# Optimization experiments

Hardware: AMD Instinct MI355X
Metric: run time of the kernel (lower is better)

## Reference

```python
import jax, jax.numpy as jnp
import numpy as np

N_ROOMS = 128
N = 2 + N_ROOMS          # 2 external wall nodes + room nodes
T = 131072               # number of evaluation times
DT = 30.0                # seconds between evaluations
Q_LIM = 500.0
K_SCALE = 1e-5           # physical scaling of sigmoid(params) -> conductances [1/s]
DAY = 86400.0
TOUT_N = 1100            # hourly outside-temperature table covering the horizon


def setup_inputs() -> dict:
    key = jax.random.key(0)
    k1, k2, k3, k4 = jax.random.split(key, 4)
    t_eval = jnp.arange(T, dtype=jnp.float32) * DT
    params = jax.random.uniform(k1, (N * N,), dtype=jnp.float32)      # torch.rand init
    heating = jax.random.normal(k2, (N_ROOMS, 3), dtype=jnp.float32)  # torch.randn init
    B = jnp.zeros((N, 1 + N_ROOMS), dtype=jnp.float32)
    B = B.at[:, 0].set(jax.random.uniform(k3, (N,), dtype=jnp.float32) * 1e-5)  # Tout coupling
    B = B.at[2:, 1:].set(jnp.eye(N_ROOMS, dtype=jnp.float32) * 1e-6)           # heat input per room
    tout_t = jnp.arange(TOUT_N, dtype=jnp.float32) * 3600.0
    tout_v = 10.0 + 5.0 * jax.random.normal(k4, (TOUT_N,), dtype=jnp.float32)
    return {"t_eval": t_eval, "params": params, "heating": heating, "B": B,
            "tout_t": tout_t, "tout_v": tout_v}


def _forward(t_eval, params, heating, B, tout_t, tout_v):
    # transform + physical scaling of parameters -> RC conductance matrix A
    theta = jax.nn.sigmoid(params) * K_SCALE
    K = theta.reshape(N, N)
    d = jnp.diag(K)
    Koff = K - jnp.diag(d)
    A = Koff - jnp.diag(Koff.sum(axis=1) + d)   # Metzler, nonpositive row sums -> stable

    # transform + heat scaling -> continuous heating profile Qrms_continuous
    Q_avg = jax.nn.sigmoid(heating[:, 0]) * Q_LIM
    phase = heating[:, 1]
    sharp = heating[:, 2]

    t0 = t_eval[0]
    te = t_eval - t0
    two_pi = 2.0 * jnp.pi

    def Tout(t):  # Tout_continuous (linear interp, like scipy interp1d)
        return jnp.interp(t + t0, tout_t, tout_v)

    def Qf(t):    # smooth periodic heating schedule per room
        return Q_avg * jax.nn.sigmoid(sharp * jnp.sin(two_pi * (t + t0) / DAY + phase))

    def f(t, x):  # dx/dt = A @ x + B @ u
        u = jnp.concatenate([Tout(t)[None], Qf(t)])[:, None]   # [1+R, 1]
        return A @ x + B @ u

    iv = (Tout(te[0]) + 4.0) * jnp.ones((N, 1), dtype=jnp.float32)

    def step(x, tt):  # one RK4 step between consecutive evaluation times
        t, dt = tt
        half = dt * 0.5
        k1 = f(t, x)
        k2 = f(t + half, x + half * k1)
        k3 = f(t + half, x + half * k2)
        k4 = f(t + dt, x + dt * k3)
        xn = x + (dt / 6.0) * (k1 + 2.0 * k2 + 2.0 * k3 + k4)
        return xn, xn

    ts = te[:-1]
    dts = te[1:] - te[:-1]
    _, xs = jax.lax.scan(step, iv, (ts, dts))
    sol = jnp.concatenate([iv[None], xs], axis=0)   # [T, N, 1]
    return sol[:, 2:]                               # room temperatures only


def reference(t_eval, params, heating, B, tout_t, tout_v):
    return _forward(t_eval, params, heating, B, tout_t, tout_v)
```

## Files before the change

kernel.cpp:

```cpp
#include <hip/hip_runtime.h>
#include <math.h>

#define NPAD 132
#define TSTEPS 131071
#define LCH 128
#define NCH 1024
#define PERIOD 2880
#define OMEGA 7.2722052166430399e-05f

#define OFF_A    0
#define OFF_A2   17160
#define OFF_A3   34320
#define OFF_M    51480
#define OFF_C1   68640
#define OFF_C2   85800
#define OFF_P1   102960
#define OFF_P2   120120
#define OFF_M2   137280
#define OFF_M4   154440
#define OFF_M64  171600
#define OFF_M128 188760
#define OFF_M2K  205920
#define OFF_C1T  223080
#define OFF_C2T  239464
#define OFF_C1B  255848
#define OFF_C2B  255978
#define OFF_C3B  256108
#define OFF_AMP  256238
#define OFF_CPH  256366
#define OFF_SPH  256494
#define OFF_SH   256622
#define OFF_W    256750
#define OFF_G    257920
#define OFF_S64  391040
#define OFF_XB   524160
#define OFF_XB2  657280
#define OFF_SA   923520
#define OFF_GP   931710
#define OFF_GP2  1306110
#define OFF_GP4  1680510
#define OFF_TT   2054910

typedef float f4 __attribute__((ext_vector_type(4)));

#define MLOAD(Q, S) asm volatile("global_load_dwordx4 %0, %1, off offset:" S \
                                 : "=v"(mr[Q]) : "v"(base))
__device__ __forceinline__ void load_mrow(const float* base, f4* mr) {
    MLOAD(0, "0");    MLOAD(1, "16");   MLOAD(2, "32");   MLOAD(3, "48");
    MLOAD(4, "64");   MLOAD(5, "80");   MLOAD(6, "96");   MLOAD(7, "112");
    MLOAD(8, "128");  MLOAD(9, "144");  MLOAD(10, "160"); MLOAD(11, "176");
    MLOAD(12, "192"); MLOAD(13, "208"); MLOAD(14, "224"); MLOAD(15, "240");
    MLOAD(16, "256"); MLOAD(17, "272"); MLOAD(18, "288"); MLOAD(19, "304");
    MLOAD(20, "320"); MLOAD(21, "336"); MLOAD(22, "352"); MLOAD(23, "368");
    MLOAD(24, "384"); MLOAD(25, "400"); MLOAD(26, "416"); MLOAD(27, "432");
    MLOAD(28, "448"); MLOAD(29, "464"); MLOAD(30, "480"); MLOAD(31, "496");
    MLOAD(32, "512");
    asm volatile("s_waitcnt vmcnt(0)" ::: "memory");
    __builtin_amdgcn_sched_barrier(0);
}

__device__ __forceinline__ float sigm(float x) { return 1.0f / (1.0f + expf(-x)); }

__device__ __forceinline__ float interp_tout(float t, const float* __restrict__ tv) {
    float u = t * (1.0f / 3600.0f);
    int idx = (int)u;
    if (idx > 1098) idx = 1098;
    float fr = u - (float)idx;
    float v0 = tv[idx];
    return v0 + fr * (tv[idx + 1] - v0);
}

__global__ __launch_bounds__(256) void build_A_kernel(
    const float* __restrict__ params, const float* __restrict__ heating,
    const float* __restrict__ Bm, const float* __restrict__ tout_v,
    float* __restrict__ ws, float* __restrict__ out) {
    const int tid = threadIdx.x;
    float* A = ws + OFF_A;

    for (int idx = tid; idx < 130 * 130; idx += 256) {
        int r = idx / 130, c = idx - r * 130;
        A[r * NPAD + c] = sigm(params[idx]) * 1e-5f;
    }
    for (int r = tid; r < 130; r += 256) { A[r * NPAD + 130] = 0.f; A[r * NPAD + 131] = 0.f; }
    __syncthreads();
    for (int r = tid; r < 130; r += 256) {
        float s = 0.0f;
        for (int k = 0; k < 130; ++k) s += A[r * NPAD + k];
        A[r * NPAD + r] = -s;
    }
    for (int i = tid; i < 128; i += 256) {
        float bd = Bm[(2 + i) * 129 + (1 + i)];
        ws[OFF_AMP + i] = sigm(heating[i * 3]) * 500.0f * bd;
        float ph = heating[i * 3 + 1];
        ws[OFF_CPH + i] = cosf(ph);
        ws[OFF_SPH + i] = sinf(ph);
        ws[OFF_SH + i]  = heating[i * 3 + 2];
    }
    float iv = tout_v[0] + 4.0f;
    for (int i = tid; i < 128; i += 256) out[i] = iv;
    for (int r = tid; r < 130; r += 256) ws[OFF_XB + r] = iv;
}

__global__ __launch_bounds__(192) void mm_kernel(float* __restrict__ ws,
                                                 int offD, int offX, int offY) {
    const float* X = ws + offX;
    const float* Y = ws + offY;
    float* dst = ws + offD;
    __shared__ float xrow[130];
    const int r = blockIdx.x;
    const int c = threadIdx.x;
    if (c < 130) xrow[c] = X[r * NPAD + c];
    __syncthreads();
    if (c < 130) {
        float acc = 0.0f;
#pragma unroll 10
        for (int k = 0; k < 130; ++k)
            acc = fmaf(xrow[k], Y[k * NPAD + c], acc);
        dst[r * NPAD + c] = acc;
    }
    if (c >= 130 && c < 132) dst[r * NPAD + c] = 0.0f;
}

__global__ __launch_bounds__(192) void mm34_kernel(float* __restrict__ ws) {
    const int b = blockIdx.x;
    const bool hi = (b >= 130);
    const int r = hi ? b - 130 : b;
    const float* X = ws + (hi ? OFF_A2 : OFF_A);
    const float* Y = ws + OFF_A2;
    float* dst = ws + (hi ? OFF_P2 : OFF_A3);
    __shared__ float xrow[130];
    const int c = threadIdx.x;
    if (c < 130) xrow[c] = X[r * NPAD + c];
    __syncthreads();
    if (c < 130) {
        float acc = 0.0f;
#pragma unroll 10
        for (int k = 0; k < 130; ++k)
            acc = fmaf(xrow[k], Y[k * NPAD + c], acc);
        dst[r * NPAD + c] = acc;
    }
    if (c >= 130 && c < 132) dst[r * NPAD + c] = 0.0f;
}

__global__ __launch_bounds__(256) void combine_kernel(float* __restrict__ ws) {
    int idx = blockIdx.x * 256 + threadIdx.x;
    if (idx >= 130 * 130) return;
    int r = idx / 130, c = idx - r * 130;
    int o = r * NPAD + c;
    const float* A  = ws + OFF_A;
    const float* A2 = ws + OFF_A2;
    const float* A3 = ws + OFF_A3;
    const float* A4 = ws + OFF_P2;
    float eye = (r == c) ? 1.0f : 0.0f;
    float a = A[o], a2 = A2[o], a3 = A3[o], a4 = A4[o];
    float c1v = 5.0f * eye + 150.0f * a + 2250.0f * a2 + 33750.0f * a3;
    float c2v = 20.0f * eye + 300.0f * a + 2250.0f * a2;
    ws[OFF_M  + o] = eye + 30.0f * a + 450.0f * a2 + 4500.0f * a3 + 33750.0f * a4;
    ws[OFF_C1 + o] = c1v;
    ws[OFF_C2 + o] = c2v;
    if (r >= 2 && c >= 2) {
        ws[OFF_C1T + (c - 2) * 128 + (r - 2)] = c1v;
        ws[OFF_C2T + (c - 2) * 128 + (r - 2)] = c2v;
    }
    if (c == 0) {
        ws[OFF_M + r * NPAD + 130] = 0.f; ws[OFF_M + r * NPAD + 131] = 0.f;
        ws[OFF_C1 + r * NPAD + 130] = 0.f; ws[OFF_C1 + r * NPAD + 131] = 0.f;
        ws[OFF_C2 + r * NPAD + 130] = 0.f; ws[OFF_C2 + r * NPAD + 131] = 0.f;
    }
}

__global__ __launch_bounds__(192) void vecs2_kernel(const float* __restrict__ Bm,
                                                    float* __restrict__ ws) {
    const int r = threadIdx.x;
    const float* C1 = ws + OFF_C1;
    const float* C2 = ws + OFF_C2;
    const float* Mm = ws + OFF_M;
    __shared__ __align__(16) float va[132], vb[132], vd[132];
    __shared__ __align__(16) float na[132], nb[132], nd[132];
    __shared__ float a1s[130], a2s[130], c1bs[130];

    if (r < 132) { va[r] = 0.f; vb[r] = 0.f; vd[r] = 0.f; na[r] = 0.f; nb[r] = 0.f; nd[r] = 0.f; }
    __syncthreads();
    if (r < 130) {
        float s1 = 0.0f, s2 = 0.0f;
        for (int k = 0; k < 130; ++k) {
            float b0 = Bm[k * 129];
            s1 = fmaf(C1[r * NPAD + k], b0, s1);
            s2 = fmaf(C2[r * NPAD + k], b0, s2);
        }
        float c3 = 5.0f * Bm[r * 129];
        ws[OFF_C1B + r] = s1; ws[OFF_C2B + r] = s2; ws[OFF_C3B + r] = c3;
        ws[OFF_W + 7 * 130 + r] = s2;
        ws[OFF_W + 8 * 130 + r] = c3;
        va[r] = s1; vb[r] = s2; vd[r] = c3; c1bs[r] = s1;
    }
    __syncthreads();

    for (int st = 1; st <= 3; ++st) {
        if (r < 130) {
            const f4* mp = reinterpret_cast<const f4*>(&Mm[r * NPAD]);
            const f4* pa = reinterpret_cast<const f4*>(va);
            const f4* pb = reinterpret_cast<const f4*>(vb);
            const f4* pd = reinterpret_cast<const f4*>(vd);
            float aa = 0.f, ab = 0.f, ad = 0.f;
#pragma unroll
            for (int q = 0; q < 33; ++q) {
                f4 m = mp[q];
                f4 xa = pa[q], xb = pb[q], xd = pd[q];
                aa = fmaf(m.x, xa.x, fmaf(m.y, xa.y, fmaf(m.z, xa.z, fmaf(m.w, xa.w, aa))));
                ab = fmaf(m.x, xb.x, fmaf(m.y, xb.y, fmaf(m.z, xb.z, fmaf(m.w, xb.w, ab))));
                ad = fmaf(m.x, xd.x, fmaf(m.y, xd.y, fmaf(m.z, xd.z, fmaf(m.w, xd.w, ad))));
            }
            na[r] = aa; nb[r] = ab; nd[r] = ad;
        }
        __syncthreads();
        if (r < 130) {
            if (st == 1) { ws[OFF_W + 5 * 130 + r] = nb[r]; ws[OFF_W + 6 * 130 + r] = nd[r] + c1bs[r]; a1s[r] = na[r]; }
            if (st == 2) { ws[OFF_W + 3 * 130 + r] = nb[r]; ws[OFF_W + 4 * 130 + r] = nd[r] + a1s[r]; a2s[r] = na[r]; }
            if (st == 3) { ws[OFF_W + 0 * 130 + r] = na[r]; ws[OFF_W + 1 * 130 + r] = nb[r]; ws[OFF_W + 2 * 130 + r] = nd[r] + a2s[r]; }
            va[r] = na[r]; vb[r] = nb[r]; vd[r] = nd[r];
        }
        __syncthreads();
    }
}

__global__ __launch_bounds__(256) void gper_kernel(float* __restrict__ ws) {
    const int tid = threadIdx.x;
    const int n0 = blockIdx.x * 32;
    const float* C1T = ws + OFF_C1T;
    const float* C2T = ws + OFF_C2T;
    const float* C1 = ws + OFF_C1;
    const float* C2 = ws + OFF_C2;
    const float* amp = ws + OFF_AMP;
    const float* cph = ws + OFF_CPH;
    const float* sph = ws + OFF_SPH;
    const float* sh  = ws + OFF_SH;
    float* P = ws + OFF_GP;

    __shared__ __align__(16) float qgT[128][36];
    __shared__ __align__(16) float qmT[128][36];
    __shared__ float sth[65], cth[65];

    for (int j = tid; j < 65; j += 256) {
        float t = (j < 33) ? (float)(n0 + j) * 30.0f
                           : (float)(n0 + j - 33) * 30.0f + 15.0f;
        float a = t * OMEGA;
        sth[j] = sinf(a);
        cth[j] = cosf(a);
    }
    __syncthreads();

    for (int p = tid; p < 65 * 128; p += 256) {
        int j = p >> 7, i = p & 127;
        float s = sth[j] * cph[i] + cth[j] * sph[i];
        float v = amp[i] / (1.0f + __expf(-sh[i] * s));
        if (j < 33) qgT[i][j] = v; else qmT[i][j - 33] = v;
    }
    __syncthreads();

    const int rr = tid & 127;
    const int half = tid >> 7;
    const int r = rr + 2;
    float acc1[16], acc2[16];
#pragma unroll
    for (int w = 0; w < 16; ++w) { acc1[w] = 0.0f; acc2[w] = 0.0f; }

    for (int k = 0; k < 128; ++k) {
        float c1 = C1T[(k << 7) + rr];
        float c2 = C2T[(k << 7) + rr];
        const float4* q1p = reinterpret_cast<const float4*>(&qgT[k][half * 16]);
        const float4* q2p = reinterpret_cast<const float4*>(&qmT[k][half * 16]);
#pragma unroll
        for (int w = 0; w < 4; ++w) {
            float4 a = q1p[w];
            float4 b = q2p[w];
            acc1[4 * w + 0] = fmaf(c1, a.x, acc1[4 * w + 0]);
            acc1[4 * w + 1] = fmaf(c1, a.y, acc1[4 * w + 1]);
            acc1[4 * w + 2] = fmaf(c1, a.z, acc1[4 * w + 2]);
            acc1[4 * w + 3] = fmaf(c1, a.w, acc1[4 * w + 3]);
            acc2[4 * w + 0] = fmaf(c2, b.x, acc2[4 * w + 0]);
            acc2[4 * w + 1] = fmaf(c2, b.y, acc2[4 * w + 1]);
            acc2[4 * w + 2] = fmaf(c2, b.z, acc2[4 * w + 2]);
            acc2[4 * w + 3] = fmaf(c2, b.w, acc2[4 * w + 3]);
        }
    }
#pragma unroll
    for (int w = 0; w < 16; ++w) {
        int n = half * 16 + w;
        P[(n0 + n) * 130 + r] = acc1[w] + acc2[w] + 5.0f * qgT[rr][n + 1];
    }

    if (tid < 64) {
        int r2 = tid >> 5;
        int n = tid & 31;
        float acc = 0.0f;
        for (int k = 0; k < 128; ++k) {
            acc = fmaf(C1[r2 * NPAD + 2 + k], qgT[k][n], acc);
            acc = fmaf(C2[r2 * NPAD + 2 + k], qmT[k][n], acc);
        }
        P[(n0 + n) * 130 + r2] = acc;
    }
}

__global__ __launch_bounds__(192) void pdouble_kernel(float* __restrict__ ws,
                                                      int offD, int offS, int offMat, int shift) {
    const int m0 = blockIdx.x * 16;
    const int tid = threadIdx.x;
    const float* S = ws + offS;
    const float* Mat = ws + offMat;
    float* D = ws + offD;
    __shared__ __align__(16) float xs2[16][132];
    for (int p = tid; p < 16 * 132; p += 192) {
        int i = p / 132, rr = p - i * 132;
        xs2[i][rr] = (rr < 130) ? S[(m0 + i) * 130 + rr] : 0.0f;
    }
    __syncthreads();
    const int r = tid;
    if (r < 130) {
        float acc[16];
#pragma unroll
        for (int i = 0; i < 16; ++i) acc[i] = 0.0f;
        const f4* mp = reinterpret_cast<const f4*>(&Mat[r * NPAD]);
        for (int q = 0; q < 33; ++q) {
            f4 m = mp[q];
#pragma unroll
            for (int i = 0; i < 16; ++i) {
                f4 x = reinterpret_cast<const f4*>(xs2[i])[q];
                acc[i] = fmaf(m.x, x.x, fmaf(m.y, x.y, fmaf(m.z, x.z, fmaf(m.w, x.w, acc[i]))));
            }
        }
#pragma unroll
        for (int i = 0; i < 16; ++i) {
            int ms = m0 + i + shift; if (ms >= PERIOD) ms -= PERIOD;
            D[(m0 + i) * 130 + r] = acc[i] + S[ms * 130 + r];
        }
    }
}

__global__ __launch_bounds__(256) void ttab_kernel(const float* __restrict__ tout_v,
                                                   float* __restrict__ ws) {
    int n = blockIdx.x * 256 + threadIdx.x;
    if (n < 131080) {
        float t = (float)n * 30.0f;
        float2* TT = reinterpret_cast<float2*>(ws + OFF_TT);
        TT[n] = make_float2(interp_tout(t, tout_v), interp_tout(t + 15.0f, tout_v));
    }
}

__global__ __launch_bounds__(192, 2) void chunk_accum_kernel(float* __restrict__ ws) {
    const int c = blockIdx.x;
    const int r = threadIdx.x;
    const float* M4 = ws + OFF_M4;
    const float* P4 = ws + OFF_GP4;
    const float2* TT = reinterpret_cast<const float2*>(ws + OFF_TT);

    __shared__ __align__(16) float xs[2][132];
    f4 mr[33];
    float w0 = 0.f, w1 = 0.f, w2 = 0.f, w3 = 0.f, w4 = 0.f, w5 = 0.f, w6 = 0.f, w7 = 0.f, w8 = 0.f;
    if (r < 130) {
        load_mrow(&M4[r * NPAD], mr);
        w0 = ws[OFF_W + 0 * 130 + r]; w1 = ws[OFF_W + 1 * 130 + r]; w2 = ws[OFF_W + 2 * 130 + r];
        w3 = ws[OFF_W + 3 * 130 + r]; w4 = ws[OFF_W + 4 * 130 + r]; w5 = ws[OFF_W + 5 * 130 + r];
        w6 = ws[OFF_W + 6 * 130 + r]; w7 = ws[OFF_W + 7 * 130 + r]; w8 = ws[OFF_W + 8 * 130 + r];
    }
    if (r < 132) { xs[0][r] = 0.0f; xs[1][r] = 0.0f; }
    __syncthreads();

    const int base = c * LCH;
    int mu = base % PERIOD;
    float pv = (r < 130) ? P4[mu * 130 + r] : 0.0f;
    int cur = 0;
    for (int u = 0; u < 32; ++u) {
        if (r < 130) {
            const int n = base + 4 * u;
            float2 t0 = TT[n], t1 = TT[n + 1], t2 = TT[n + 2], t3 = TT[n + 3];
            float tg4 = TT[n + 4].x;
            float gcur = pv
                + t0.x * w0 + t0.y * w1 + t1.x * w2 + t1.y * w3
                + t2.x * w4 + t2.y * w5 + t3.x * w6 + t3.y * w7 + tg4 * w8;
            mu = (mu + 4 >= PERIOD) ? mu + 4 - PERIOD : mu + 4;
            if (u + 1 < 32) pv = P4[mu * 130 + r];
            const f4* xp = reinterpret_cast<const f4*>(xs[cur]);
            float a0 = 0.f, a1 = 0.f, a2 = 0.f, a3 = 0.f;
#pragma unroll
            for (int q = 0; q < 33; ++q) {
                f4 xv = xp[q];
                a0 = fmaf(mr[q].x, xv.x, a0);
                a1 = fmaf(mr[q].y, xv.y, a1);
                a2 = fmaf(mr[q].z, xv.z, a2);
                a3 = fmaf(mr[q].w, xv.w, a3);
            }
            float val = (a0 + a1) + (a2 + a3) + gcur;
            xs[cur ^ 1][r] = val;
            if (u == 15) ws[OFF_S64 + c * 130 + r] = val;
        }
        __syncthreads();
        cur ^= 1;
    }
    if (r < 130) ws[OFF_G + c * 130 + r] = xs[cur][r];
}

__global__ __launch_bounds__(192, 2) void superaccum_kernel(float* __restrict__ ws) {
    const int s = blockIdx.x;
    const int r = threadIdx.x;
    const float* MP = ws + OFF_M128;
    const float* G = ws + OFF_G;

    __shared__ __align__(16) float xs[2][132];
    f4 mr[33];
    if (r < 130) load_mrow(&MP[r * NPAD], mr);
    if (r < 132) { xs[0][r] = 0.0f; xs[1][r] = 0.0f; }
    __syncthreads();

    int cur = 0;
    for (int i = 0; i < 16; ++i) {
        if (r < 130) {
            const f4* xp = reinterpret_cast<const f4*>(xs[cur]);
            float a0 = 0.f, a1 = 0.f, a2 = 0.f, a3 = 0.f;
#pragma unroll
            for (int q = 0; q < 33; ++q) {
                f4 xv = xp[q];
                a0 = fmaf(mr[q].x, xv.x, a0);
                a1 = fmaf(mr[q].y, xv.y, a1);
                a2 = fmaf(mr[q].z, xv.z, a2);
                a3 = fmaf(mr[q].w, xv.w, a3);
            }
            xs[cur ^ 1][r] = (a0 + a1) + (a2 + a3) + G[(16 * s + i) * 130 + r];
        }
        __syncthreads();
        cur ^= 1;
    }
    if (r < 130) ws[OFF_SA + s * 130 + r] = xs[cur][r];
}

__global__ __launch_bounds__(192, 2) void superbound_kernel(float* __restrict__ ws) {
    const int r = threadIdx.x;
    const float* M2K = ws + OFF_M2K;
    const float* SA = ws + OFF_SA;
    float* xb = ws + OFF_XB;

    __shared__ __align__(16) float xs[2][132];
    f4 mr[33];
    if (r < 130) load_mrow(&M2K[r * NPAD], mr);
    if (r < 132) { xs[0][r] = (r < 130) ? xb[r] : 0.0f; xs[1][r] = 0.0f; }
    __syncthreads();

    int cur = 0;
    for (int s = 0; s < 63; ++s) {
        if (r < 130) {
            const f4* xp = reinterpret_cast<const f4*>(xs[cur]);
            float a0 = 0.f, a1 = 0.f, a2 = 0.f, a3 = 0.f;
#pragma unroll
            for (int q = 0; q < 33; ++q) {
                f4 xv = xp[q];
                a0 = fmaf(mr[q].x, xv.x, a0);
                a1 = fmaf(mr[q].y, xv.y, a1);
                a2 = fmaf(mr[q].z, xv.z, a2);
                a3 = fmaf(mr[q].w, xv.w, a3);
            }
            float val = (a0 + a1) + (a2 + a3) + SA[s * 130 + r];
            xs[cur ^ 1][r] = val;
            xb[(16 * s + 16) * 130 + r] = val;
        }
        __syncthreads();
        cur ^= 1;
    }
}

__global__ __launch_bounds__(192, 2) void chunkbound_kernel(float* __restrict__ ws) {
    const int s = blockIdx.x;
    const int r = threadIdx.x;
    const float* MP = ws + OFF_M128;
    const float* G = ws + OFF_G;
    float* xb = ws + OFF_XB;

    __shared__ __align__(16) float xs[2][132];
    f4 mr[33];
    if (r < 130) load_mrow(&MP[r * NPAD], mr);
    if (r < 132) { xs[0][r] = (r < 130) ? xb[(16 * s) * 130 + r] : 0.0f; xs[1][r] = 0.0f; }
    __syncthreads();

    int cur = 0;
    for (int i = 0; i < 15; ++i) {
        if (r < 130) {
            const f4* xp = reinterpret_cast<const f4*>(xs[cur]);
            float a0 = 0.f, a1 = 0.f, a2 = 0.f, a3 = 0.f;
#pragma unroll
            for (int q = 0; q < 33; ++q) {
                f4 xv = xp[q];
                a0 = fmaf(mr[q].x, xv.x, a0);
                a1 = fmaf(mr[q].y, xv.y, a1);
                a2 = fmaf(mr[q].z, xv.z, a2);
                a3 = fmaf(mr[q].w, xv.w, a3);
            }
            float val = (a0 + a1) + (a2 + a3) + G[(16 * s + i) * 130 + r];
            xs[cur ^ 1][r] = val;
            xb[(16 * s + i + 1) * 130 + r] = val;
        }
        __syncthreads();
        cur ^= 1;
    }
}

__global__ __launch_bounds__(192, 2) void subbound_kernel(float* __restrict__ ws) {
    const int c = blockIdx.x;
    const int r = threadIdx.x;
    const float* M64 = ws + OFF_M64;
    const float* xb = ws + OFF_XB;
    float* xb2 = ws + OFF_XB2;

    __shared__ __align__(16) float xs[132];
    if (r < 132) xs[r] = (r < 130) ? xb[c * 130 + r] : 0.0f;
    __syncthreads();
    if (r < 130) {
        const f4* xp = reinterpret_cast<const f4*>(xs);
        const f4* mp = reinterpret_cast<const f4*>(&M64[r * NPAD]);
        float a0 = 0.f, a1 = 0.f, a2 = 0.f, a3 = 0.f;
#pragma unroll
        for (int q = 0; q < 33; ++q) {
            f4 m = mp[q];
            f4 xv = xp[q];
            a0 = fmaf(m.x, xv.x, a0);
            a1 = fmaf(m.y, xv.y, a1);
            a2 = fmaf(m.z, xv.z, a2);
            a3 = fmaf(m.w, xv.w, a3);
        }
        xb2[(2 * c) * 130 + r] = xs[r];
        xb2[(2 * c + 1) * 130 + r] = (a0 + a1) + (a2 + a3) + ws[OFF_S64 + c * 130 + r];
    }
}

__global__ __launch_bounds__(192, 2) void chunk_emit_kernel(float* __restrict__ ws,
                                                            float* __restrict__ out) {
    const int ec = blockIdx.x;
    const int r = threadIdx.x;
    const float* Mm = ws + OFF_M;
    const float* P = ws + OFF_GP;
    const float2* TT = reinterpret_cast<const float2*>(ws + OFF_TT);
    const float* xb2 = ws + OFF_XB2;

    __shared__ __align__(16) float xs[2][132];
    f4 mr[33];
    float c1br = 0.f, c2br = 0.f, c3br = 0.f;
    if (r < 130) {
        load_mrow(&Mm[r * NPAD], mr);
        c1br = ws[OFF_C1B + r]; c2br = ws[OFF_C2B + r]; c3br = ws[OFF_C3B + r];
    }
    if (r < 132) { xs[0][r] = (r < 130) ? xb2[ec * 130 + r] : 0.0f; xs[1][r] = 0.0f; }
    __syncthreads();

    const int base = ec * 64;
    const int len = min(64, TSTEPS - base);
    int m = base % PERIOD;
    float pv = (r < 130) ? P[m * 130 + r] : 0.0f;
    float2 tc = TT[base], tn = TT[base + 1];
    int cur = 0;
    for (int j = 0; j < len; ++j) {
        if (r < 130) {
            float gcur = pv + tc.x * c1br + tc.y * c2br + tn.x * c3br;
            m = (m + 1 == PERIOD) ? 0 : m + 1;
            if (j + 1 < len) { pv = P[m * 130 + r]; tc = tn; tn = TT[base + j + 2]; }
            const f4* xp = reinterpret_cast<const f4*>(xs[cur]);
            float a0 = 0.f, a1 = 0.f, a2 = 0.f, a3 = 0.f;
#pragma unroll
            for (int q = 0; q < 33; ++q) {
                f4 xv = xp[q];
                a0 = fmaf(mr[q].x, xv.x, a0);
                a1 = fmaf(mr[q].y, xv.y, a1);
                a2 = fmaf(mr[q].z, xv.z, a2);
                a3 = fmaf(mr[q].w, xv.w, a3);
            }
            float val = (a0 + a1) + (a2 + a3) + gcur;
            xs[cur ^ 1][r] = val;
            if (r >= 2) out[(base + j + 1) * 128 + (r - 2)] = val;
        }
        __syncthreads();
        cur ^= 1;
    }
}

extern "C" void kernel_launch(void* const* d_in, const int* in_sizes, int n_in,
                              void* d_out, int out_size, void* d_ws, size_t ws_size,
                              hipStream_t stream) {
    const float* params  = (const float*)d_in[1];
    const float* heating = (const float*)d_in[2];
    const float* Bm      = (const float*)d_in[3];
    const float* tout_v  = (const float*)d_in[5];
    float* out = (float*)d_out;
    float* ws = (float*)d_ws;

    build_A_kernel<<<1, 256, 0, stream>>>(params, heating, Bm, tout_v, ws, out);

    mm_kernel<<<130, 192, 0, stream>>>(ws, OFF_A2, OFF_A, OFF_A);
    mm34_kernel<<<260, 192, 0, stream>>>(ws);
    combine_kernel<<<67, 256, 0, stream>>>(ws);
    vecs2_kernel<<<1, 192, 0, stream>>>(Bm, ws);
    gper_kernel<<<90, 256, 0, stream>>>(ws);
    ttab_kernel<<<513, 256, 0, stream>>>(tout_v, ws);

    mm_kernel<<<130, 192, 0, stream>>>(ws, OFF_M2,   OFF_M,    OFF_M);
    mm_kernel<<<130, 192, 0, stream>>>(ws, OFF_M4,   OFF_M2,   OFF_M2);
    mm_kernel<<<130, 192, 0, stream>>>(ws, OFF_P1,   OFF_M4,   OFF_M4);
    mm_kernel<<<130, 192, 0, stream>>>(ws, OFF_P2,   OFF_P1,   OFF_P1);
    mm_kernel<<<130, 192, 0, stream>>>(ws, OFF_P1,   OFF_P2,   OFF_P2);
    mm_kernel<<<130, 192, 0, stream>>>(ws, OFF_M64,  OFF_P1,   OFF_P1);
    mm_kernel<<<130, 192, 0, stream>>>(ws, OFF_M128, OFF_M64,  OFF_M64);
    mm_kernel<<<130, 192, 0, stream>>>(ws, OFF_P1,   OFF_M128, OFF_M128);
    mm_kernel<<<130, 192, 0, stream>>>(ws, OFF_P2,   OFF_P1,   OFF_P1);
    mm_kernel<<<130, 192, 0, stream>>>(ws, OFF_P1,   OFF_P2,   OFF_P2);
    mm_kernel<<<130, 192, 0, stream>>>(ws, OFF_M2K,  OFF_P1,   OFF_P1);

    pdouble_kernel<<<180, 192, 0, stream>>>(ws, OFF_GP2, OFF_GP,  OFF_M,  1);
    pdouble_kernel<<<180, 192, 0, stream>>>(ws, OFF_GP4, OFF_GP2, OFF_M2, 2);

    chunk_accum_kernel<<<NCH, 192, 0, stream>>>(ws);
    superaccum_kernel<<<63, 192, 0, stream>>>(ws);
    superbound_kernel<<<1, 192, 0, stream>>>(ws);
    chunkbound_kernel<<<64, 192, 0, stream>>>(ws);
    subbound_kernel<<<NCH, 192, 0, stream>>>(ws);
    chunk_emit_kernel<<<2 * NCH, 192, 0, stream>>>(ws, out);
}
```

Baseline: 505.2 us.

## Fuse setup and scan launches into persistent kernels with atomic grid barriers

Replaces the long chain of small setup kernels (A build, matrix powers, combine, vector prep, eleven squaring matmuls) and the three scan-level kernels with a few persistent kernels that step between phases through an atomic-counter grid barrier. The goal is to remove per-launch overhead and idle gaps between dependent tiny launches. The cost is a spin-wait barrier whose correctness depends on all blocks being co-resident, plus a memset to reset the counters. The scan kernel also drops the register-preloaded matrix rows in favour of direct vector loads.

```diff
diff --git a/kernel.cpp b/kernel.cpp
--- a/kernel.cpp
+++ b/kernel.cpp
@@ -40,6 +40,7 @@
 #define OFF_GP2  1306110
 #define OFF_GP4  1680510
 #define OFF_TT   2054910
+#define OFF_CNT  2317072
 
 typedef float f4 __attribute__((ext_vector_type(4)));
 
@@ -59,6 +60,17 @@
     __builtin_amdgcn_sched_barrier(0);
 }
 
+__device__ __forceinline__ void gridbar(unsigned* cnt, unsigned target) {
+    __syncthreads();
+    if (threadIdx.x == 0) {
+        __threadfence();
+        atomicAdd(cnt, 1u);
+        while (atomicAdd(cnt, 0u) < target) __builtin_amdgcn_s_sleep(2);
+        __threadfence();
+    }
+    __syncthreads();
+}
+
 __device__ __forceinline__ float sigm(float x) { return 1.0f / (1.0f + expf(-x)); }
 
 __device__ __forceinline__ float interp_tout(float t, const float* __restrict__ tv) {
@@ -70,157 +82,159 @@
     return v0 + fr * (tv[idx + 1] - v0);
 }
 
-__global__ __launch_bounds__(256) void build_A_kernel(
+__global__ __launch_bounds__(192) void prep1_kernel(
     const float* __restrict__ params, const float* __restrict__ heating,
     const float* __restrict__ Bm, const float* __restrict__ tout_v,
-    float* __restrict__ ws, float* __restrict__ out) {
-    const int tid = threadIdx.x;
+    float* __restrict__ ws, float* __restrict__ out, unsigned* cnt) {
+    const int r = blockIdx.x;
+    const int c = threadIdx.x;
     float* A = ws + OFF_A;
-
-    for (int idx = tid; idx < 130 * 130; idx += 256) {
-        int r = idx / 130, c = idx - r * 130;
-        A[r * NPAD + c] = sigm(params[idx]) * 1e-5f;
-    }
-    for (int r = tid; r < 130; r += 256) { A[r * NPAD + 130] = 0.f; A[r * NPAD + 131] = 0.f; }
-    __syncthreads();
-    for (int r = tid; r < 130; r += 256) {
+    __shared__ __align__(16) float xrow[132];
+    __shared__ __align__(16) float yrow[132];
+    __shared__ __align__(16) float va[132], vb[132], vd[132];
+    __shared__ __align__(16) float na[132], nb[132], nd[132];
+    __shared__ float a1s[130], a2s[130], c1bs[130];
+
+    if (c < 130) A[r * NPAD + c] = sigm(params[r * 130 + c]) * 1e-5f;
+    if (c >= 130 && c < 132) A[r * NPAD + c] = 0.0f;
+    __syncthreads();
+    if (c == 0) {
         float s = 0.0f;
         for (int k = 0; k < 130; ++k) s += A[r * NPAD + k];
         A[r * NPAD + r] = -s;
     }
-    for (int i = tid; i < 128; i += 256) {
-        float bd = Bm[(2 + i) * 129 + (1 + i)];
-        ws[OFF_AMP + i] = sigm(heating[i * 3]) * 500.0f * bd;
-        float ph = heating[i * 3 + 1];
-        ws[OFF_CPH + i] = cosf(ph);
-        ws[OFF_SPH + i] = sinf(ph);
-        ws[OFF_SH + i]  = heating[i * 3 + 2];
-    }
-    float iv = tout_v[0] + 4.0f;
-    for (int i = tid; i < 128; i += 256) out[i] = iv;
-    for (int r = tid; r < 130; r += 256) ws[OFF_XB + r] = iv;
-}
-
-__global__ __launch_bounds__(192) void mm_kernel(float* __restrict__ ws,
-                                                 int offD, int offX, int offY) {
-    const float* X = ws + offX;
-    const float* Y = ws + offY;
-    float* dst = ws + offD;
-    __shared__ float xrow[130];
-    const int r = blockIdx.x;
-    const int c = threadIdx.x;
-    if (c < 130) xrow[c] = X[r * NPAD + c];
+    if (r == 0) {
+        if (c < 128) {
+            float bd = Bm[(2 + c) * 129 + (1 + c)];
+            ws[OFF_AMP + c] = sigm(heating[c * 3]) * 500.0f * bd;
+            float ph = heating[c * 3 + 1];
+            ws[OFF_CPH + c] = cosf(ph);
+            ws[OFF_SPH + c] = sinf(ph);
+            ws[OFF_SH + c]  = heating[c * 3 + 2];
+        }
+        float iv = tout_v[0] + 4.0f;
+        if (c < 128) out[c] = iv;
+        if (c < 130) ws[OFF_XB + c] = iv;
+    }
+    gridbar(cnt, 130u * 1);
+
+    if (c < 132) xrow[c] = A[r * NPAD + c];
     __syncthreads();
     if (c < 130) {
         float acc = 0.0f;
 #pragma unroll 10
-        for (int k = 0; k < 130; ++k)
-            acc = fmaf(xrow[k], Y[k * NPAD + c], acc);
-        dst[r * NPAD + c] = acc;
-    }
-    if (c >= 130 && c < 132) dst[r * NPAD + c] = 0.0f;
-}
-
-__global__ __launch_bounds__(192) void mm34_kernel(float* __restrict__ ws) {
-    const int b = blockIdx.x;
-    const bool hi = (b >= 130);
-    const int r = hi ? b - 130 : b;
-    const float* X = ws + (hi ? OFF_A2 : OFF_A);
-    const float* Y = ws + OFF_A2;
-    float* dst = ws + (hi ? OFF_P2 : OFF_A3);
-    __shared__ float xrow[130];
+        for (int k = 0; k < 130; ++k) acc = fmaf(xrow[k], A[k * NPAD + c], acc);
+        ws[OFF_A2 + r * NPAD + c] = acc;
+    } else if (c < 132) ws[OFF_A2 + r * NPAD + c] = 0.0f;
+    gridbar(cnt, 130u * 2);
+
+    if (c < 132) yrow[c] = ws[OFF_A2 + r * NPAD + c];
+    __syncthreads();
+    if (c < 130) {
+        float a3 = 0.0f, a4 = 0.0f;
+#pragma unroll 5
+        for (int k = 0; k < 130; ++k) {
+            float a2kc = ws[OFF_A2 + k * NPAD + c];
+            a3 = fmaf(xrow[k], a2kc, a3);
+            a4 = fmaf(yrow[k], a2kc, a4);
+        }
+        ws[OFF_A3 + r * NPAD + c] = a3;
+        ws[OFF_P2 + r * NPAD + c] = a4;
+    } else if (c < 132) { ws[OFF_A3 + r * NPAD + c] = 0.0f; ws[OFF_P2 + r * NPAD + c] = 0.0f; }
+    gridbar(cnt, 130u * 3);
+
+    if (c < 130) {
+        int o = r * NPAD + c;
+        float eye = (r == c) ? 1.0f : 0.0f;
+        float a = A[o], a2 = ws[OFF_A2 + o], a3 = ws[OFF_A3 + o], a4 = ws[OFF_P2 + o];
+        float c1v = 5.0f * eye + 150.0f * a + 2250.0f * a2 + 33750.0f * a3;
+        float c2v = 20.0f * eye + 300.0f * a + 2250.0f * a2;
+        ws[OFF_M  + o] = eye + 30.0f * a + 450.0f * a2 + 4500.0f * a3 + 33750.0f * a4;
+        ws[OFF_C1 + o] = c1v;
+        ws[OFF_C2 + o] = c2v;
+        if (r >= 2 && c >= 2) {
+            ws[OFF_C1T + (c - 2) * 128 + (r - 2)] = c1v;
+            ws[OFF_C2T + (c - 2) * 128 + (r - 2)] = c2v;
+        }
+    } else if (c < 132) {
+        ws[OFF_M + r * NPAD + c] = 0.0f;
+        ws[OFF_C1 + r * NPAD + c] = 0.0f;
+        ws[OFF_C2 + r * NPAD + c] = 0.0f;
+    }
+    gridbar(cnt, 130u * 4);
+
+    if (r == 0) {
+        const float* C1 = ws + OFF_C1;
+        const float* C2 = ws + OFF_C2;
+        const float* Mm = ws + OFF_M;
+        if (c < 132) { va[c] = 0.f; vb[c] = 0.f; vd[c] = 0.f; na[c] = 0.f; nb[c] = 0.f; nd[c] = 0.f; }
+        __syncthreads();
+        if (c < 130) {
+            float s1 = 0.0f, s2 = 0.0f;
+            for (int k = 0; k < 130; ++k) {
+                float b0 = Bm[k * 129];
+                s1 = fmaf(C1[c * NPAD + k], b0, s1);
+                s2 = fmaf(C2[c * NPAD + k], b0, s2);
+            }
+            float c3 = 5.0f * Bm[c * 129];
+            ws[OFF_C1B + c] = s1; ws[OFF_C2B + c] = s2; ws[OFF_C3B + c] = c3;
+            ws[OFF_W + 7 * 130 + c] = s2;
+            ws[OFF_W + 8 * 130 + c] = c3;
+            va[c] = s1; vb[c] = s2; vd[c] = c3; c1bs[c] = s1;
+        }
+        __syncthreads();
+        for (int st = 1; st <= 3; ++st) {
+            if (c < 130) {
+                const f4* mp = reinterpret_cast<const f4*>(&Mm[c * NPAD]);
+                const f4* pa = reinterpret_cast<const f4*>(va);
+                const f4* pb = reinterpret_cast<const f4*>(vb);
+                const f4* pd = reinterpret_cast<const f4*>(vd);
+                float aa = 0.f, ab = 0.f, ad = 0.f;
+#pragma unroll
+                for (int q = 0; q < 33; ++q) {
+                    f4 m = mp[q];
+                    f4 xa = pa[q], xb = pb[q], xd = pd[q];
+                    aa = fmaf(m.x, xa.x, fmaf(m.y, xa.y, fmaf(m.z, xa.z, fmaf(m.w, xa.w, aa))));
+                    ab = fmaf(m.x, xb.x, fmaf(m.y, xb.y, fmaf(m.z, xb.z, fmaf(m.w, xb.w, ab))));
+                    ad = fmaf(m.x, xd.x, fmaf(m.y, xd.y, fmaf(m.z, xd.z, fmaf(m.w, xd.w, ad))));
+                }
+                na[c] = aa; nb[c] = ab; nd[c] = ad;
+            }
+            __syncthreads();
+            if (c < 130) {
+                if (st == 1) { ws[OFF_W + 5 * 130 + c] = nb[c]; ws[OFF_W + 6 * 130 + c] = nd[c] + c1bs[c]; a1s[c] = na[c]; }
+                if (st == 2) { ws[OFF_W + 3 * 130 + c] = nb[c]; ws[OFF_W + 4 * 130 + c] = nd[c] + a1s[c]; a2s[c] = na[c]; }
+                if (st == 3) { ws[OFF_W + 0 * 130 + c] = na[c]; ws[OFF_W + 1 * 130 + c] = nb[c]; ws[OFF_W + 2 * 130 + c] = nd[c] + a2s[c]; }
+                va[c] = na[c]; vb[c] = nb[c]; vd[c] = nd[c];
+            }
+            __syncthreads();
+        }
+    }
+}
+
+__global__ __launch_bounds__(192) void prep2_kernel(float* __restrict__ ws,
+                                                    unsigned* cnt) {
+    const int r = blockIdx.x;
     const int c = threadIdx.x;
-    if (c < 130) xrow[c] = X[r * NPAD + c];
-    __syncthreads();
-    if (c < 130) {
-        float acc = 0.0f;
+    __shared__ __align__(16) float xrow[132];
+    constexpr int SRC[11] = {OFF_M, OFF_M2, OFF_M4, OFF_P1, OFF_P2, OFF_P1,
+                             OFF_M64, OFF_M128, OFF_P1, OFF_P2, OFF_P1};
+    constexpr int DST[11] = {OFF_M2, OFF_M4, OFF_P1, OFF_P2, OFF_P1, OFF_M64,
+                             OFF_M128, OFF_P1, OFF_P2, OFF_P1, OFF_M2K};
+#pragma unroll
+    for (int p = 0; p < 11; ++p) {
+        const float* S = ws + SRC[p];
+        float* D = ws + DST[p];
+        if (c < 132) xrow[c] = S[r * NPAD + c];
+        __syncthreads();
+        if (c < 130) {
+            float acc = 0.0f;
 #pragma unroll 10
-        for (int k = 0; k < 130; ++k)
-            acc = fmaf(xrow[k], Y[k * NPAD + c], acc);
-        dst[r * NPAD + c] = acc;
-    }
-    if (c >= 130 && c < 132) dst[r * NPAD + c] = 0.0f;
-}
-
-__global__ __launch_bounds__(256) void combine_kernel(float* __restrict__ ws) {
-    int idx = blockIdx.x * 256 + threadIdx.x;
-    if (idx >= 130 * 130) return;
-    int r = idx / 130, c = idx - r * 130;
-    int o = r * NPAD + c;
-    const float* A  = ws + OFF_A;
-    const float* A2 = ws + OFF_A2;
-    const float* A3 = ws + OFF_A3;
-    const float* A4 = ws + OFF_P2;
-    float eye = (r == c) ? 1.0f : 0.0f;
-    float a = A[o], a2 = A2[o], a3 = A3[o], a4 = A4[o];
-    float c1v = 5.0f * eye + 150.0f * a + 2250.0f * a2 + 33750.0f * a3;
-    float c2v = 20.0f * eye + 300.0f * a + 2250.0f * a2;
-    ws[OFF_M  + o] = eye + 30.0f * a + 450.0f * a2 + 4500.0f * a3 + 33750.0f * a4;
-    ws[OFF_C1 + o] = c1v;
-    ws[OFF_C2 + o] = c2v;
-    if (r >= 2 && c >= 2) {
-        ws[OFF_C1T + (c - 2) * 128 + (r - 2)] = c1v;
-        ws[OFF_C2T + (c - 2) * 128 + (r - 2)] = c2v;
-    }
-    if (c == 0) {
-        ws[OFF_M + r * NPAD + 130] = 0.f; ws[OFF_M + r * NPAD + 131] = 0.f;
-        ws[OFF_C1 + r * NPAD + 130] = 0.f; ws[OFF_C1 + r * NPAD + 131] = 0.f;
-        ws[OFF_C2 + r * NPAD + 130] = 0.f; ws[OFF_C2 + r * NPAD + 131] = 0.f;
-    }
-}
-
-__global__ __launch_bounds__(192) void vecs2_kernel(const float* __restrict__ Bm,
-                                                    float* __restrict__ ws) {
-    const int r = threadIdx.x;
-    const float* C1 = ws + OFF_C1;
-    const float* C2 = ws + OFF_C2;
-    const float* Mm = ws + OFF_M;
-    __shared__ __align__(16) float va[132], vb[132], vd[132];
-    __shared__ __align__(16) float na[132], nb[132], nd[132];
-    __shared__ float a1s[130], a2s[130], c1bs[130];
-
-    if (r < 132) { va[r] = 0.f; vb[r] = 0.f; vd[r] = 0.f; na[r] = 0.f; nb[r] = 0.f; nd[r] = 0.f; }
-    __syncthreads();
-    if (r < 130) {
-        float s1 = 0.0f, s2 = 0.0f;
-        for (int k = 0; k < 130; ++k) {
-            float b0 = Bm[k * 129];
-            s1 = fmaf(C1[r * NPAD + k], b0, s1);
-            s2 = fmaf(C2[r * NPAD + k], b0, s2);
-        }
-        float c3 = 5.0f * Bm[r * 129];
-        ws[OFF_C1B + r] = s1; ws[OFF_C2B + r] = s2; ws[OFF_C3B + r] = c3;
-        ws[OFF_W + 7 * 130 + r] = s2;
-        ws[OFF_W + 8 * 130 + r] = c3;
-        va[r] = s1; vb[r] = s2; vd[r] = c3; c1bs[r] = s1;
-    }
-    __syncthreads();
-
-    for (int st = 1; st <= 3; ++st) {
-        if (r < 130) {
-            const f4* mp = reinterpret_cast<const f4*>(&Mm[r * NPAD]);
-            const f4* pa = reinterpret_cast<const f4*>(va);
-            const f4* pb = reinterpret_cast<const f4*>(vb);
-            const f4* pd = reinterpret_cast<const f4*>(vd);
-            float aa = 0.f, ab = 0.f, ad = 0.f;
-#pragma unroll
-            for (int q = 0; q < 33; ++q) {
-                f4 m = mp[q];
-                f4 xa = pa[q], xb = pb[q], xd = pd[q];
-                aa = fmaf(m.x, xa.x, fmaf(m.y, xa.y, fmaf(m.z, xa.z, fmaf(m.w, xa.w, aa))));
-                ab = fmaf(m.x, xb.x, fmaf(m.y, xb.y, fmaf(m.z, xb.z, fmaf(m.w, xb.w, ab))));
-                ad = fmaf(m.x, xd.x, fmaf(m.y, xd.y, fmaf(m.z, xd.z, fmaf(m.w, xd.w, ad))));
-            }
-            na[r] = aa; nb[r] = ab; nd[r] = ad;
-        }
-        __syncthreads();
-        if (r < 130) {
-            if (st == 1) { ws[OFF_W + 5 * 130 + r] = nb[r]; ws[OFF_W + 6 * 130 + r] = nd[r] + c1bs[r]; a1s[r] = na[r]; }
-            if (st == 2) { ws[OFF_W + 3 * 130 + r] = nb[r]; ws[OFF_W + 4 * 130 + r] = nd[r] + a1s[r]; a2s[r] = na[r]; }
-            if (st == 3) { ws[OFF_W + 0 * 130 + r] = na[r]; ws[OFF_W + 1 * 130 + r] = nb[r]; ws[OFF_W + 2 * 130 + r] = nd[r] + a2s[r]; }
-            va[r] = na[r]; vb[r] = nb[r]; vd[r] = nd[r];
-        }
-        __syncthreads();
+            for (int k = 0; k < 130; ++k)
+                acc = fmaf(xrow[k], S[k * NPAD + c], acc);
+            D[r * NPAD + c] = acc;
+        } else if (c < 132) D[r * NPAD + c] = 0.0f;
+        if (p < 10) gridbar(cnt, 130u * (p + 1));
     }
 }
 
@@ -400,109 +414,98 @@
     if (r < 130) ws[OFF_G + c * 130 + r] = xs[cur][r];
 }
 
-__global__ __launch_bounds__(192, 2) void superaccum_kernel(float* __restrict__ ws) {
-    const int s = blockIdx.x;
+__global__ __launch_bounds__(192) void scan3_kernel(float* __restrict__ ws,
+                                                    unsigned* cnt) {
+    const int b = blockIdx.x;
     const int r = threadIdx.x;
-    const float* MP = ws + OFF_M128;
-    const float* G = ws + OFF_G;
-
-    __shared__ __align__(16) float xs[2][132];
-    f4 mr[33];
-    if (r < 130) load_mrow(&MP[r * NPAD], mr);
-    if (r < 132) { xs[0][r] = 0.0f; xs[1][r] = 0.0f; }
-    __syncthreads();
-
-    int cur = 0;
-    for (int i = 0; i < 16; ++i) {
-        if (r < 130) {
-            const f4* xp = reinterpret_cast<const f4*>(xs[cur]);
-            float a0 = 0.f, a1 = 0.f, a2 = 0.f, a3 = 0.f;
-#pragma unroll
-            for (int q = 0; q < 33; ++q) {
-                f4 xv = xp[q];
-                a0 = fmaf(mr[q].x, xv.x, a0);
-                a1 = fmaf(mr[q].y, xv.y, a1);
-                a2 = fmaf(mr[q].z, xv.z, a2);
-                a3 = fmaf(mr[q].w, xv.w, a3);
-            }
-            xs[cur ^ 1][r] = (a0 + a1) + (a2 + a3) + G[(16 * s + i) * 130 + r];
-        }
-        __syncthreads();
-        cur ^= 1;
-    }
-    if (r < 130) ws[OFF_SA + s * 130 + r] = xs[cur][r];
-}
-
-__global__ __launch_bounds__(192, 2) void superbound_kernel(float* __restrict__ ws) {
-    const int r = threadIdx.x;
-    const float* M2K = ws + OFF_M2K;
-    const float* SA = ws + OFF_SA;
-    float* xb = ws + OFF_XB;
-
-    __shared__ __align__(16) float xs[2][132];
-    f4 mr[33];
-    if (r < 130) load_mrow(&M2K[r * NPAD], mr);
-    if (r < 132) { xs[0][r] = (r < 130) ? xb[r] : 0.0f; xs[1][r] = 0.0f; }
-    __syncthreads();
-
-    int cur = 0;
-    for (int s = 0; s < 63; ++s) {
-        if (r < 130) {
-            const f4* xp = reinterpret_cast<const f4*>(xs[cur]);
-            float a0 = 0.f, a1 = 0.f, a2 = 0.f, a3 = 0.f;
-#pragma unroll
-            for (int q = 0; q < 33; ++q) {
-                f4 xv = xp[q];
-                a0 = fmaf(mr[q].x, xv.x, a0);
-                a1 = fmaf(mr[q].y, xv.y, a1);
-                a2 = fmaf(mr[q].z, xv.z, a2);
-                a3 = fmaf(mr[q].w, xv.w, a3);
-            }
-            float val = (a0 + a1) + (a2 + a3) + SA[s * 130 + r];
-            xs[cur ^ 1][r] = val;
-            xb[(16 * s + 16) * 130 + r] = val;
-        }
-        __syncthreads();
-        cur ^= 1;
-    }
-}
-
-__global__ __launch_bounds__(192, 2) void chunkbound_kernel(float* __restrict__ ws) {
-    const int s = blockIdx.x;
-    const int r = threadIdx.x;
-    const float* MP = ws + OFF_M128;
     const float* G = ws + OFF_G;
     float* xb = ws + OFF_XB;
-
     __shared__ __align__(16) float xs[2][132];
-    f4 mr[33];
-    if (r < 130) load_mrow(&MP[r * NPAD], mr);
-    if (r < 132) { xs[0][r] = (r < 130) ? xb[(16 * s) * 130 + r] : 0.0f; xs[1][r] = 0.0f; }
-    __syncthreads();
-
-    int cur = 0;
-    for (int i = 0; i < 15; ++i) {
-        if (r < 130) {
-            const f4* xp = reinterpret_cast<const f4*>(xs[cur]);
-            float a0 = 0.f, a1 = 0.f, a2 = 0.f, a3 = 0.f;
-#pragma unroll
-            for (int q = 0; q < 33; ++q) {
-                f4 xv = xp[q];
-                a0 = fmaf(mr[q].x, xv.x, a0);
-                a1 = fmaf(mr[q].y, xv.y, a1);
-                a2 = fmaf(mr[q].z, xv.z, a2);
-                a3 = fmaf(mr[q].w, xv.w, a3);
-            }
-            float val = (a0 + a1) + (a2 + a3) + G[(16 * s + i) * 130 + r];
-            xs[cur ^ 1][r] = val;
-            xb[(16 * s + i + 1) * 130 + r] = val;
-        }
+
+    if (r < 132) { xs[0][r] = 0.0f; xs[1][r] = 0.0f; }
+    __syncthreads();
+    if (b < 63) {
+        const f4* mp = reinterpret_cast<const f4*>(&ws[OFF_M128 + (r < 130 ? r : 0) * NPAD]);
+        int cur = 0;
+        for (int i = 0; i < 16; ++i) {
+            if (r < 130) {
+                const f4* xp = reinterpret_cast<const f4*>(xs[cur]);
+                float a0 = 0.f, a1 = 0.f, a2 = 0.f, a3 = 0.f;
+#pragma unroll
+                for (int q = 0; q < 33; ++q) {
+                    f4 m = mp[q];
+                    f4 xv = xp[q];
+                    a0 = fmaf(m.x, xv.x, a0);
+                    a1 = fmaf(m.y, xv.y, a1);
+                    a2 = fmaf(m.z, xv.z, a2);
+                    a3 = fmaf(m.w, xv.w, a3);
+                }
+                xs[cur ^ 1][r] = (a0 + a1) + (a2 + a3) + G[(16 * b + i) * 130 + r];
+            }
+            __syncthreads();
+            cur ^= 1;
+        }
+        if (r < 130) ws[OFF_SA + b * 130 + r] = xs[cur][r];
+    }
+    gridbar(cnt, 64u);
+
+    if (b == 0) {
+        if (r < 132) { xs[0][r] = (r < 130) ? xb[r] : 0.0f; xs[1][r] = 0.0f; }
         __syncthreads();
-        cur ^= 1;
-    }
-}
-
-__global__ __launch_bounds__(192, 2) void subbound_kernel(float* __restrict__ ws) {
+        const f4* mp = reinterpret_cast<const f4*>(&ws[OFF_M2K + (r < 130 ? r : 0) * NPAD]);
+        int cur = 0;
+        for (int s = 0; s < 63; ++s) {
+            if (r < 130) {
+                const f4* xp = reinterpret_cast<const f4*>(xs[cur]);
+                float a0 = 0.f, a1 = 0.f, a2 = 0.f, a3 = 0.f;
+#pragma unroll
+                for (int q = 0; q < 33; ++q) {
+                    f4 m = mp[q];
+                    f4 xv = xp[q];
+                    a0 = fmaf(m.x, xv.x, a0);
+                    a1 = fmaf(m.y, xv.y, a1);
+                    a2 = fmaf(m.z, xv.z, a2);
+                    a3 = fmaf(m.w, xv.w, a3);
+                }
+                float val = (a0 + a1) + (a2 + a3) + ws[OFF_SA + s * 130 + r];
+                xs[cur ^ 1][r] = val;
+                xb[(16 * s + 16) * 130 + r] = val;
+            }
+            __syncthreads();
+            cur ^= 1;
+        }
+    }
+    gridbar(cnt, 128u);
+
+    if (r < 132) { xs[0][r] = (r < 130) ? xb[(16 * b) * 130 + r] : 0.0f; xs[1][r] = 0.0f; }
+    __syncthreads();
+    {
+        const f4* mp = reinterpret_cast<const f4*>(&ws[OFF_M128 + (r < 130 ? r : 0) * NPAD]);
+        int cur = 0;
+        for (int i = 0; i < 15; ++i) {
+            if (r < 130) {
+                const f4* xp = reinterpret_cast<const f4*>(xs[cur]);
+                float a0 = 0.f, a1 = 0.f, a2 = 0.f, a3 = 0.f;
+#pragma unroll
+                for (int q = 0; q < 33; ++q) {
+                    f4 m = mp[q];
+                    f4 xv = xp[q];
+                    a0 = fmaf(m.x, xv.x, a0);
+                    a1 = fmaf(m.y, xv.y, a1);
+                    a2 = fmaf(m.z, xv.z, a2);
+                    a3 = fmaf(m.w, xv.w, a3);
+                }
+                float val = (a0 + a1) + (a2 + a3) + G[(16 * b + i) * 130 + r];
+                xs[cur ^ 1][r] = val;
+                xb[(16 * b + i + 1) * 130 + r] = val;
+            }
+            __syncthreads();
+            cur ^= 1;
+        }
+    }
+}
+
+__global__ __launch_bounds__(192) void subbound_kernel(float* __restrict__ ws) {
     const int c = blockIdx.x;
     const int r = threadIdx.x;
     const float* M64 = ws + OFF_M64;
@@ -588,35 +591,20 @@
     const float* tout_v  = (const float*)d_in[5];
     float* out = (float*)d_out;
     float* ws = (float*)d_ws;
-
-    build_A_kernel<<<1, 256, 0, stream>>>(params, heating, Bm, tout_v, ws, out);
-
-    mm_kernel<<<130, 192, 0, stream>>>(ws, OFF_A2, OFF_A, OFF_A);
-    mm34_kernel<<<260, 192, 0, stream>>>(ws);
-    combine_kernel<<<67, 256, 0, stream>>>(ws);
-    vecs2_kernel<<<1, 192, 0, stream>>>(Bm, ws);
+    unsigned* cnt = (unsigned*)((float*)d_ws + OFF_CNT);
+
+    hipMemsetAsync((void*)cnt, 0, 3 * sizeof(unsigned), stream);
+
+    prep1_kernel<<<130, 192, 0, stream>>>(params, heating, Bm, tout_v, ws, out, cnt);
+    ttab_kernel<<<513, 256, 0, stream>>>(tout_v, ws);
     gper_kernel<<<90, 256, 0, stream>>>(ws);
-    ttab_kernel<<<513, 256, 0, stream>>>(tout_v, ws);
-
-    mm_kernel<<<130, 192, 0, stream>>>(ws, OFF_M2,   OFF_M,    OFF_M);
-    mm_kernel<<<130, 192, 0, stream>>>(ws, OFF_M4,   OFF_M2,   OFF_M2);
-    mm_kernel<<<130, 192, 0, stream>>>(ws, OFF_P1,   OFF_M4,   OFF_M4);
-    mm_kernel<<<130, 192, 0, stream>>>(ws, OFF_P2,   OFF_P1,   OFF_P1);
-    mm_kernel<<<130, 192, 0, stream>>>(ws, OFF_P1,   OFF_P2,   OFF_P2);
-    mm_kernel<<<130, 192, 0, stream>>>(ws, OFF_M64,  OFF_P1,   OFF_P1);
-    mm_kernel<<<130, 192, 0, stream>>>(ws, OFF_M128, OFF_M64,  OFF_M64);
-    mm_kernel<<<130, 192, 0, stream>>>(ws, OFF_P1,   OFF_M128, OFF_M128);
-    mm_kernel<<<130, 192, 0, stream>>>(ws, OFF_P2,   OFF_P1,   OFF_P1);
-    mm_kernel<<<130, 192, 0, stream>>>(ws, OFF_P1,   OFF_P2,   OFF_P2);
-    mm_kernel<<<130, 192, 0, stream>>>(ws, OFF_M2K,  OFF_P1,   OFF_P1);
+    prep2_kernel<<<130, 192, 0, stream>>>(ws, cnt + 1);
 
     pdouble_kernel<<<180, 192, 0, stream>>>(ws, OFF_GP2, OFF_GP,  OFF_M,  1);
     pdouble_kernel<<<180, 192, 0, stream>>>(ws, OFF_GP4, OFF_GP2, OFF_M2, 2);
 
     chunk_accum_kernel<<<NCH, 192, 0, stream>>>(ws);
-    superaccum_kernel<<<63, 192, 0, stream>>>(ws);
-    superbound_kernel<<<1, 192, 0, stream>>>(ws);
-    chunkbound_kernel<<<64, 192, 0, stream>>>(ws);
+    scan3_kernel<<<64, 192, 0, stream>>>(ws, cnt + 2);
     subbound_kernel<<<NCH, 192, 0, stream>>>(ws);
     chunk_emit_kernel<<<2 * NCH, 192, 0, stream>>>(ws, out);
 }
```

Result: slower. 655.4 us (+29.7%).
